# Kernel optimization log

Measured on AMD Instinct MI355X. Metric: run time of the kernel, lower is better.

The kernel has to match this reference:

```python
import math
import jax, jax.numpy as jnp
import numpy as np

EMBED_DIM = 1024
NUM_HEADS = 16
HEAD_DIM = EMBED_DIM // NUM_HEADS


def setup_inputs() -> dict:
    key = jax.random.key(0)
    ks = jax.random.split(key, 10)
    B, S, E = 2, 2048, EMBED_DIM
    x = jax.random.normal(ks[0], (B, S, E), dtype=jnp.float32)
    mask = jax.random.randint(ks[1], (B, S), 0, 2, dtype=jnp.int32)
    s = 1.0 / math.sqrt(E)
    Wq = jax.random.normal(ks[2], (E, E), dtype=jnp.float32) * s
    bq = jnp.zeros((E,), dtype=jnp.float32)
    Wk = jax.random.normal(ks[3], (E, E), dtype=jnp.float32) * s
    bk = jnp.zeros((E,), dtype=jnp.float32)
    Wv = jax.random.normal(ks[4], (E, E), dtype=jnp.float32) * s
    bv = jnp.zeros((E,), dtype=jnp.float32)
    Wo = jax.random.normal(ks[5], (E, E), dtype=jnp.float32) * s
    bo = jnp.zeros((E,), dtype=jnp.float32)
    return {"x": x, "mask": mask, "Wq": Wq, "bq": bq, "Wk": Wk, "bk": bk,
            "Wv": Wv, "bv": bv, "Wo": Wo, "bo": bo}


def reference(x, mask, Wq, bq, Wk, bk, Wv, bv, Wo, bo):
    B, S, E = x.shape
    H, D = NUM_HEADS, HEAD_DIM
    scale = math.sqrt(D)  # ScaledDotProductAttention built with head_dim

    def split_heads(t):
        return t.reshape(B, S, H, D).transpose(0, 2, 1, 3)  # [B,H,S,D]

    q = split_heads(x @ Wq + bq)
    k = split_heads(x @ Wk + bk)
    v = split_heads(x @ Wv + bv)

    scores = jnp.einsum('bhqd,bhkd->bhqk', q, k) / scale  # [B,H,S,S]
    m = mask[:, None, None, :].astype(scores.dtype)        # [B,1,1,S]
    neg = jnp.finfo(scores.dtype).min
    scores = jnp.where(m == 0, neg, scores)
    aw = jax.nn.softmax(scores, axis=-1)
    # post-softmax mask renormalization (as in the torch module)
    aw = aw * m
    denom = aw.sum(axis=-1, keepdims=True)
    aw = jnp.where(denom > 0, aw / jnp.where(denom > 0, denom, 1.0), 0.0)

    ctx = jnp.einsum('bhqk,bhkd->bhqd', aw, v)             # [B,H,S,D]
    ctx = ctx.transpose(0, 2, 1, 3).reshape(B, S, E)
    out = ctx @ Wo + bo
    return out
```

## Files before the change

### kernel.cpp

```cpp
#include <hip/hip_runtime.h>

typedef _Float16 half8 __attribute__((ext_vector_type(8)));
typedef _Float16 half4v __attribute__((ext_vector_type(4)));
typedef _Float16 h2 __attribute__((ext_vector_type(2)));
typedef float f4 __attribute__((ext_vector_type(4)));

#define ASYNC_COPY16(ldsp, gp)                                                     \
  __builtin_amdgcn_global_load_lds((__attribute__((address_space(1))) void*)(gp),  \
                                   (__attribute__((address_space(3))) void*)(ldsp),\
                                   16, 0, 0)

__device__ __forceinline__ f4 mfma16(half8 a, half8 b, f4 c) {
  return __builtin_amdgcn_mfma_f32_16x16x32_f16(a, b, c, 0, 0, 0);
}

__device__ __forceinline__ h2 pack2(float a, float b) {
  return __builtin_bit_cast(h2, __builtin_amdgcn_cvt_pkrtz(a, b));
}

#if defined(__has_builtin)
#if __has_builtin(__builtin_amdgcn_exp2f)
#define EXP2(x) __builtin_amdgcn_exp2f(x)
#endif
#if __has_builtin(__builtin_amdgcn_fdot2)
#define FDOT2(a, b, c) __builtin_amdgcn_fdot2((a), (b), (c), false)
#endif
#endif
#ifndef EXP2
#define EXP2(x) __expf((x) * 0.69314718056f)
#endif
#define KSCALE 0.18033688011f
#define FIXMAX 10.0f


__global__ __launch_bounds__(256) void k_cvt_x(const float* __restrict__ x,
                                               _Float16* __restrict__ xh) {
  int i = (blockIdx.x * 256 + threadIdx.x) * 4;
  f4 v = *(const f4*)(x + i);
  half4v h;
  h[0] = (_Float16)v[0]; h[1] = (_Float16)v[1];
  h[2] = (_Float16)v[2]; h[3] = (_Float16)v[3];
  *(half4v*)(xh + i) = h;
}

__global__ __launch_bounds__(256) void k_transpose_w(
    const float* __restrict__ Wq, const float* __restrict__ Wk,
    const float* __restrict__ Wv, const float* __restrict__ Wo,
    _Float16* __restrict__ wqkvT, _Float16* __restrict__ woT) {
  __shared__ float tw[32][33];
  int z = blockIdx.z;
  const float* w = (z == 0) ? Wq : (z == 1) ? Wk : (z == 2) ? Wv : Wo;
  _Float16* wt = (z == 3) ? woT : wqkvT + (size_t)z * 1048576;
  int k0 = blockIdx.y * 32, n0 = blockIdx.x * 32;
  int tx = threadIdx.x, ty = threadIdx.y;
  for (int j = 0; j < 32; j += 8) tw[ty + j][tx] = w[(size_t)(k0 + ty + j) * 1024 + n0 + tx];
  __syncthreads();
  for (int j = 0; j < 32; j += 8)
    wt[(size_t)(n0 + ty + j) * 1024 + k0 + tx] = (_Float16)tw[tx][ty + j];
}

__global__ __launch_bounds__(256) void k_gemm_proj(
    const _Float16* __restrict__ A, const _Float16* __restrict__ Bt,
    const float* __restrict__ bq, const float* __restrict__ bk, const float* __restrict__ bv,
    _Float16* __restrict__ Qo, _Float16* __restrict__ Ko, _Float16* __restrict__ Vto) {
  __shared__ __align__(16) _Float16 As[128 * 32];
  __shared__ __align__(16) _Float16 Bs[128 * 32];
  const int t = threadIdx.x, lane = t & 63, w = t >> 6;
  const int qd = lane >> 4, lr = lane & 15;
  const int m0 = blockIdx.y * 128, n0 = blockIdx.x * 128;
  const int wm = (w & 1) * 64, wn = (w >> 1) * 64;
  const f4 z4 = {0.f, 0.f, 0.f, 0.f};
  f4 acc[4][4];
#pragma unroll
  for (int i = 0; i < 4; ++i)
#pragma unroll
    for (int j = 0; j < 4; ++j) acc[i][j] = z4;

  const int c0 = t, c1 = t + 256;
  for (int k0 = 0; k0 < 1024; k0 += 32) {
    const _Float16* ga0 = A + (size_t)(m0 + (c0 >> 2)) * 1024 + k0 + (c0 & 3) * 8;
    const _Float16* ga1 = A + (size_t)(m0 + (c1 >> 2)) * 1024 + k0 + (c1 & 3) * 8;
    const _Float16* gb0 = Bt + (size_t)(n0 + (c0 >> 2)) * 1024 + k0 + (c0 & 3) * 8;
    const _Float16* gb1 = Bt + (size_t)(n0 + (c1 >> 2)) * 1024 + k0 + (c1 & 3) * 8;
    char* la = (char*)As + w * 1024;
    char* lb = (char*)Bs + w * 1024;
    ASYNC_COPY16(la, ga0);
    ASYNC_COPY16(la + 4096, ga1);
    ASYNC_COPY16(lb, gb0);
    ASYNC_COPY16(lb + 4096, gb1);
    __syncthreads();
    half8 af[4], bf[4];
#pragma unroll
    for (int i = 0; i < 4; ++i)
      af[i] = *(const half8*)(As + (wm + i * 16 + lr) * 32 + qd * 8);
#pragma unroll
    for (int j = 0; j < 4; ++j)
      bf[j] = *(const half8*)(Bs + (wn + j * 16 + lr) * 32 + qd * 8);
#pragma unroll
    for (int i = 0; i < 4; ++i)
#pragma unroll
      for (int j = 0; j < 4; ++j) acc[i][j] = mfma16(af[i], bf[j], acc[i][j]);
    __syncthreads();
  }

  const int mat = n0 >> 10;
  const float* bias = (mat == 0) ? bq : (mat == 1) ? bk : bv;
  if (mat == 2) {
#pragma unroll
    for (int i = 0; i < 4; ++i)
#pragma unroll
      for (int j = 0; j < 4; ++j) {
        int n = (n0 + wn + j * 16 + lr) & 1023;
        int hh = n >> 6, d = n & 63;
        int mb = m0 + wm + i * 16 + qd * 4;
        int bb = mb >> 11, sb = mb & 2047;
        float bval = bias[n];
        half4v hv;
#pragma unroll
        for (int r = 0; r < 4; ++r) hv[r] = (_Float16)(acc[i][j][r] + bval);
        *(half4v*)(Vto + ((size_t)(bb * 16 + hh) * 64 + d) * 2048 + sb) = hv;
      }
  } else {
    _Float16* outp = (mat == 0) ? Qo : Ko;
    const float scl = (mat == 0) ? KSCALE : 1.f;
#pragma unroll
    for (int i = 0; i < 4; ++i)
#pragma unroll
      for (int j = 0; j < 4; ++j)
#pragma unroll
        for (int r = 0; r < 4; ++r) {
          int m = m0 + wm + i * 16 + qd * 4 + r;
          int n = (n0 + wn + j * 16 + lr) & 1023;
          float v = (acc[i][j][r] + bias[n]) * scl;
          int bb = m >> 11, s = m & 2047, hh = n >> 6, d = n & 63;
          outp[(size_t)((bb * 16 + hh) * 2048 + s) * 64 + d] = (_Float16)v;
        }
  }
}

__global__ __launch_bounds__(256, 2) void k_attn(
    const _Float16* __restrict__ Qg, const _Float16* __restrict__ Kg,
    const _Float16* __restrict__ Vtg, const int* __restrict__ maskg,
    _Float16* __restrict__ Op, float* __restrict__ ml) {
  __shared__ __align__(16) _Float16 Ks[64][72];
  __shared__ __align__(16) _Float16 Vts[64][72];
  __shared__ __align__(16) _Float16 Pq[4][16][72];
  __shared__ float Msk[64];

  const int bh = blockIdx.y;
  const int b = bh >> 4;
  const int q0 = blockIdx.x * 128;
  const int z = blockIdx.z;
  const int kb = z * 1024;
  const int t = threadIdx.x, lane = t & 63, w = t >> 6;
  const int qd = lane >> 4, lr = lane & 15;

  half8 qf[2][2];
#pragma unroll
  for (int rt = 0; rt < 2; ++rt)
#pragma unroll
    for (int ks = 0; ks < 2; ++ks)
      qf[rt][ks] = *(const half8*)(Qg + (size_t)(bh * 2048 + q0 + w * 32 + rt * 16 + lr) * 64 +
                                   ks * 32 + qd * 8);

  float l_i[2] = {0.f, 0.f};
  const f4 z4 = {0.f, 0.f, 0.f, 0.f};
  f4 O[2][4];
#pragma unroll
  for (int rt = 0; rt < 2; ++rt)
#pragma unroll
    for (int dt = 0; dt < 4; ++dt) O[rt][dt] = z4;

  const int sr0 = t >> 3, scc = (t & 7) * 8;
  const int sr1 = sr0 + 32;
  const _Float16* Kbase = Kg + (size_t)bh * 2048 * 64 + (size_t)kb * 64;
  const _Float16* Vtbase = Vtg + (size_t)bh * 64 * 2048 + kb;

  f4 kr0 = *(const f4*)(Kbase + (size_t)sr0 * 64 + scc);
  f4 kr1 = *(const f4*)(Kbase + (size_t)sr1 * 64 + scc);
  f4 vr0 = *(const f4*)(Vtbase + (size_t)sr0 * 2048 + scc);
  f4 vr1 = *(const f4*)(Vtbase + (size_t)sr1 * 2048 + scc);
  float mval = 0.f;
  if (t < 64) mval = maskg[b * 2048 + kb + t] ? -FIXMAX : -30010.f;

#if defined(FDOT2)
  const h2 one2 = {(_Float16)1.f, (_Float16)1.f};
#endif

  for (int it = 0; it < 16; ++it) {
    __syncthreads();
    *(f4*)&Ks[sr0][scc] = kr0;
    *(f4*)&Ks[sr1][scc] = kr1;
    *(f4*)&Vts[sr0][scc] = vr0;
    *(f4*)&Vts[sr1][scc] = vr1;
    if (t < 64) Msk[t] = mval;
    __syncthreads();

    if (it < 15) {
      int kk = (it + 1) * 64;
      kr0 = *(const f4*)(Kbase + (size_t)(kk + sr0) * 64 + scc);
      kr1 = *(const f4*)(Kbase + (size_t)(kk + sr1) * 64 + scc);
      vr0 = *(const f4*)(Vtbase + (size_t)sr0 * 2048 + kk + scc);
      vr1 = *(const f4*)(Vtbase + (size_t)sr1 * 2048 + kk + scc);
      if (t < 64) mval = maskg[b * 2048 + kb + kk + t] ? -FIXMAX : -30010.f;
    }

    f4 sc[2][4];
#pragma unroll
    for (int kt = 0; kt < 4; ++kt) {
      f4 mv = *(const f4*)&Msk[kt * 16 + qd * 4];
      sc[0][kt] = mv;
      sc[1][kt] = mv;
    }
#pragma unroll
    for (int kt = 0; kt < 4; ++kt) {
      half8 k0 = *(const half8*)&Ks[kt * 16 + lr][qd * 8];
      half8 k1 = *(const half8*)&Ks[kt * 16 + lr][32 + qd * 8];
      sc[0][kt] = mfma16(k0, qf[0][0], sc[0][kt]);
      sc[0][kt] = mfma16(k1, qf[0][1], sc[0][kt]);
      sc[1][kt] = mfma16(k0, qf[1][0], sc[1][kt]);
      sc[1][kt] = mfma16(k1, qf[1][1], sc[1][kt]);
    }

#pragma unroll
    for (int rt = 0; rt < 2; ++rt) {
      float s = 0.f;
#pragma unroll
      for (int kt = 0; kt < 4; ++kt) {
        float p0 = EXP2(sc[rt][kt][0]);
        float p1 = EXP2(sc[rt][kt][1]);
        float p2 = EXP2(sc[rt][kt][2]);
        float p3 = EXP2(sc[rt][kt][3]);
        h2 pa = pack2(p0, p1);
        h2 pb = pack2(p2, p3);
#if defined(FDOT2)
        s = FDOT2(pa, one2, s);
        s = FDOT2(pb, one2, s);
#else
        s += p0 + p1 + p2 + p3;
#endif
        half4v hv;
        hv.lo = pa;
        hv.hi = pb;
        *(half4v*)&Pq[w][lr][kt * 16 + qd * 4] = hv;
      }
      s += __shfl_xor(s, 16, 64);
      s += __shfl_xor(s, 32, 64);
      l_i[rt] += s;

      half8 bp0 = *(const half8*)&Pq[w][lr][qd * 8];
      half8 bp1 = *(const half8*)&Pq[w][lr][32 + qd * 8];
#pragma unroll
      for (int dt = 0; dt < 4; ++dt) {
        half8 va0 = *(const half8*)&Vts[dt * 16 + lr][qd * 8];
        half8 va1 = *(const half8*)&Vts[dt * 16 + lr][32 + qd * 8];
        O[rt][dt] = mfma16(va0, bp0, O[rt][dt]);
        O[rt][dt] = mfma16(va1, bp1, O[rt][dt]);
      }
    }
  }

#pragma unroll
  for (int rt = 0; rt < 2; ++rt) {
    int qrow = q0 + w * 32 + rt * 16 + lr;
    size_t rowi = (size_t)(z * 32 + bh) * 2048 + qrow;
    _Float16* op = Op + rowi * 64;
#pragma unroll
    for (int dt = 0; dt < 4; ++dt) {
      half4v hv;
#pragma unroll
      for (int r = 0; r < 4; ++r) hv[r] = (_Float16)O[rt][dt][r];
      *(half4v*)(op + dt * 16 + qd * 4) = hv;
    }
    if (qd == 0) ml[rowi] = l_i[rt];
  }
}

__global__ __launch_bounds__(256) void k_merge(const _Float16* __restrict__ Op,
                                               const float* __restrict__ ml,
                                               _Float16* __restrict__ ctx) {
  int idx = blockIdx.x * 256 + threadIdx.x;
  int d8 = (idx & 7) * 8;
  int h = (idx >> 3) & 15;
  int q = idx >> 7;
  int b = q >> 11, s = q & 2047;
  int bh = b * 16 + h;
  size_t r1 = (size_t)bh * 2048 + s;
  size_t r2 = (size_t)(32 + bh) * 2048 + s;
  float l1 = ml[r1], l2 = ml[r2];
  float inv = 1.f / fmaxf(l1 + l2, 1e-20f);
  half8 o1 = *(const half8*)(Op + r1 * 64 + d8);
  half8 o2 = *(const half8*)(Op + r2 * 64 + d8);
  half8 ho;
#pragma unroll
  for (int j = 0; j < 8; ++j)
    ho[j] = (_Float16)(((float)o1[j] + (float)o2[j]) * inv);
  *(half8*)(ctx + (size_t)q * 1024 + h * 64 + d8) = ho;
}

__global__ __launch_bounds__(256) void k_gemm_out(
    const _Float16* __restrict__ A, const _Float16* __restrict__ Bt,
    const float* __restrict__ bo, float* __restrict__ out) {
  __shared__ __align__(16) _Float16 As[64 * 32];
  __shared__ __align__(16) _Float16 Bs[128 * 32];
  const int t = threadIdx.x, lane = t & 63, w = t >> 6;
  const int qd = lane >> 4, lr = lane & 15;
  const int m0 = blockIdx.y * 64, n0 = blockIdx.x * 128;
  const int wm = (w & 1) * 32, wn = (w >> 1) * 64;
  const f4 z4 = {0.f, 0.f, 0.f, 0.f};
  f4 acc[2][4];
#pragma unroll
  for (int i = 0; i < 2; ++i)
#pragma unroll
    for (int j = 0; j < 4; ++j) acc[i][j] = z4;

  const int c0 = t, c1 = t + 256;
  for (int k0 = 0; k0 < 1024; k0 += 32) {
    const _Float16* ga = A + (size_t)(m0 + (t >> 2)) * 1024 + k0 + (t & 3) * 8;
    const _Float16* gb0 = Bt + (size_t)(n0 + (c0 >> 2)) * 1024 + k0 + (c0 & 3) * 8;
    const _Float16* gb1 = Bt + (size_t)(n0 + (c1 >> 2)) * 1024 + k0 + (c1 & 3) * 8;
    char* la = (char*)As + w * 1024;
    char* lb = (char*)Bs + w * 1024;
    ASYNC_COPY16(la, ga);
    ASYNC_COPY16(lb, gb0);
    ASYNC_COPY16(lb + 4096, gb1);
    __syncthreads();
    half8 af[2], bf[4];
#pragma unroll
    for (int i = 0; i < 2; ++i)
      af[i] = *(const half8*)(As + (wm + i * 16 + lr) * 32 + qd * 8);
#pragma unroll
    for (int j = 0; j < 4; ++j)
      bf[j] = *(const half8*)(Bs + (wn + j * 16 + lr) * 32 + qd * 8);
#pragma unroll
    for (int i = 0; i < 2; ++i)
#pragma unroll
      for (int j = 0; j < 4; ++j) acc[i][j] = mfma16(af[i], bf[j], acc[i][j]);
    __syncthreads();
  }
#pragma unroll
  for (int i = 0; i < 2; ++i)
#pragma unroll
    for (int j = 0; j < 4; ++j)
#pragma unroll
      for (int r = 0; r < 4; ++r) {
        int m = m0 + wm + i * 16 + qd * 4 + r;
        int n = n0 + wn + j * 16 + lr;
        out[(size_t)m * 1024 + n] = acc[i][j][r] + bo[n];
      }
}

extern "C" void kernel_launch(void* const* d_in, const int* in_sizes, int n_in,
                              void* d_out, int out_size, void* d_ws, size_t ws_size,
                              hipStream_t stream) {
  const float* x = (const float*)d_in[0];
  const int* mask = (const int*)d_in[1];
  const float* Wq = (const float*)d_in[2];
  const float* bq = (const float*)d_in[3];
  const float* Wk = (const float*)d_in[4];
  const float* bk = (const float*)d_in[5];
  const float* Wv = (const float*)d_in[6];
  const float* bv = (const float*)d_in[7];
  const float* Wo = (const float*)d_in[8];
  const float* bo = (const float*)d_in[9];
  float* out = (float*)d_out;
  char* ws = (char*)d_ws;
  const size_t MB = 1 << 20;

  _Float16* Oph   = (_Float16*)(ws + 0);
  _Float16* xh    = (_Float16*)(ws + 0);
  _Float16* wqkvT = (_Float16*)(ws + 8 * MB);
  _Float16* woT   = (_Float16*)(ws + 16 * MB);
  _Float16* Qh    = (_Float16*)(ws + 18 * MB);
  _Float16* ctxh  = (_Float16*)(ws + 18 * MB);
  _Float16* Kh    = (_Float16*)(ws + 26 * MB);
  _Float16* Vth   = (_Float16*)(ws + 34 * MB);
  float*    mlw   = (float*)   (ws + 42 * MB);

  k_cvt_x<<<dim3(4096), dim3(256), 0, stream>>>(x, xh);
  k_transpose_w<<<dim3(32, 32, 4), dim3(32, 8), 0, stream>>>(Wq, Wk, Wv, Wo, wqkvT, woT);
  k_gemm_proj<<<dim3(24, 32), dim3(256), 0, stream>>>(xh, wqkvT, bq, bk, bv, Qh, Kh, Vth);
  k_attn<<<dim3(16, 32, 2), dim3(256), 0, stream>>>(Qh, Kh, Vth, mask, Oph, mlw);
  k_merge<<<dim3(2048), dim3(256), 0, stream>>>(Oph, mlw, ctxh);
  k_gemm_out<<<dim3(8, 64), dim3(256), 0, stream>>>(ctxh, woT, bo, out);
}
```

Measured before the change: 205.8 us.

## Double attention query tile per block and merge prep kernels into one launch

Each attention workgroup now handles 256 query rows (64 per wave) instead of 128, so every K/V tile staged into LDS is reused across twice as many queries. This halves K/V global loads and the grid size. The x-conversion and weight-transpose kernels are also fused into a single launch to save one kernel launch. In exchange the attention grid drops to 512 blocks, which may underfill the GPU, and register pressure rises with the larger O accumulator.

Result: no change. 203.5 us (-1.1%).

```diff
diff --git a/kernel.cpp b/kernel.cpp
--- a/kernel.cpp
+++ b/kernel.cpp
@@ -33,26 +33,28 @@
 #define FIXMAX 10.0f
 
 
-__global__ __launch_bounds__(256) void k_cvt_x(const float* __restrict__ x,
-                                               _Float16* __restrict__ xh) {
-  int i = (blockIdx.x * 256 + threadIdx.x) * 4;
-  f4 v = *(const f4*)(x + i);
-  half4v h;
-  h[0] = (_Float16)v[0]; h[1] = (_Float16)v[1];
-  h[2] = (_Float16)v[2]; h[3] = (_Float16)v[3];
-  *(half4v*)(xh + i) = h;
-}
-
-__global__ __launch_bounds__(256) void k_transpose_w(
+__global__ __launch_bounds__(256) void k_prep(
+    const float* __restrict__ x, _Float16* __restrict__ xh,
     const float* __restrict__ Wq, const float* __restrict__ Wk,
     const float* __restrict__ Wv, const float* __restrict__ Wo,
     _Float16* __restrict__ wqkvT, _Float16* __restrict__ woT) {
   __shared__ float tw[32][33];
-  int z = blockIdx.z;
+  const int bid = blockIdx.x, t = threadIdx.x;
+  if (bid < 4096) {
+    int i = (bid * 256 + t) * 4;
+    f4 v = *(const f4*)(x + i);
+    half4v h;
+    h[0] = (_Float16)v[0]; h[1] = (_Float16)v[1];
+    h[2] = (_Float16)v[2]; h[3] = (_Float16)v[3];
+    *(half4v*)(xh + i) = h;
+    return;
+  }
+  const int idx = bid - 4096;
+  const int z = idx >> 10, rem = idx & 1023;
+  const int n0 = (rem & 31) * 32, k0 = (rem >> 5) * 32;
   const float* w = (z == 0) ? Wq : (z == 1) ? Wk : (z == 2) ? Wv : Wo;
   _Float16* wt = (z == 3) ? woT : wqkvT + (size_t)z * 1048576;
-  int k0 = blockIdx.y * 32, n0 = blockIdx.x * 32;
-  int tx = threadIdx.x, ty = threadIdx.y;
+  const int tx = t & 31, ty = t >> 5;
   for (int j = 0; j < 32; j += 8) tw[ty + j][tx] = w[(size_t)(k0 + ty + j) * 1024 + n0 + tx];
   __syncthreads();
   for (int j = 0; j < 32; j += 8)
@@ -149,25 +151,25 @@
 
   const int bh = blockIdx.y;
   const int b = bh >> 4;
-  const int q0 = blockIdx.x * 128;
+  const int q0 = blockIdx.x * 256;
   const int z = blockIdx.z;
   const int kb = z * 1024;
   const int t = threadIdx.x, lane = t & 63, w = t >> 6;
   const int qd = lane >> 4, lr = lane & 15;
 
-  half8 qf[2][2];
-#pragma unroll
-  for (int rt = 0; rt < 2; ++rt)
+  half8 qf[4][2];
+#pragma unroll
+  for (int rt = 0; rt < 4; ++rt)
 #pragma unroll
     for (int ks = 0; ks < 2; ++ks)
-      qf[rt][ks] = *(const half8*)(Qg + (size_t)(bh * 2048 + q0 + w * 32 + rt * 16 + lr) * 64 +
+      qf[rt][ks] = *(const half8*)(Qg + (size_t)(bh * 2048 + q0 + w * 64 + rt * 16 + lr) * 64 +
                                    ks * 32 + qd * 8);
 
-  float l_i[2] = {0.f, 0.f};
+  float l_i[4] = {0.f, 0.f, 0.f, 0.f};
   const f4 z4 = {0.f, 0.f, 0.f, 0.f};
-  f4 O[2][4];
-#pragma unroll
-  for (int rt = 0; rt < 2; ++rt)
+  f4 O[4][4];
+#pragma unroll
+  for (int rt = 0; rt < 4; ++rt)
 #pragma unroll
     for (int dt = 0; dt < 4; ++dt) O[rt][dt] = z4;
 
@@ -205,64 +207,69 @@
       if (t < 64) mval = maskg[b * 2048 + kb + kk + t] ? -FIXMAX : -30010.f;
     }
 
-    f4 sc[2][4];
-#pragma unroll
-    for (int kt = 0; kt < 4; ++kt) {
-      f4 mv = *(const f4*)&Msk[kt * 16 + qd * 4];
-      sc[0][kt] = mv;
-      sc[1][kt] = mv;
+#pragma unroll
+    for (int rtp = 0; rtp < 2; ++rtp) {
+      const int r0 = rtp * 2, r1 = rtp * 2 + 1;
+      f4 sc[2][4];
+#pragma unroll
+      for (int kt = 0; kt < 4; ++kt) {
+        f4 mv = *(const f4*)&Msk[kt * 16 + qd * 4];
+        sc[0][kt] = mv;
+        sc[1][kt] = mv;
+      }
+#pragma unroll
+      for (int kt = 0; kt < 4; ++kt) {
+        half8 k0 = *(const half8*)&Ks[kt * 16 + lr][qd * 8];
+        half8 k1 = *(const half8*)&Ks[kt * 16 + lr][32 + qd * 8];
+        sc[0][kt] = mfma16(k0, qf[r0][0], sc[0][kt]);
+        sc[0][kt] = mfma16(k1, qf[r0][1], sc[0][kt]);
+        sc[1][kt] = mfma16(k0, qf[r1][0], sc[1][kt]);
+        sc[1][kt] = mfma16(k1, qf[r1][1], sc[1][kt]);
+      }
+
+#pragma unroll
+      for (int rr = 0; rr < 2; ++rr) {
+        const int rt = rtp * 2 + rr;
+        float s = 0.f;
+#pragma unroll
+        for (int kt = 0; kt < 4; ++kt) {
+          float p0 = EXP2(sc[rr][kt][0]);
+          float p1 = EXP2(sc[rr][kt][1]);
+          float p2 = EXP2(sc[rr][kt][2]);
+          float p3 = EXP2(sc[rr][kt][3]);
+          h2 pa = pack2(p0, p1);
+          h2 pb = pack2(p2, p3);
+#if defined(FDOT2)
+          s = FDOT2(pa, one2, s);
+          s = FDOT2(pb, one2, s);
+#else
+          s += p0 + p1 + p2 + p3;
+#endif
+          half4v hv;
+          hv.lo = pa;
+          hv.hi = pb;
+          *(half4v*)&Pq[w][lr][kt * 16 + qd * 4] = hv;
+        }
+        s += __shfl_xor(s, 16, 64);
+        s += __shfl_xor(s, 32, 64);
+        l_i[rt] += s;
+
+        half8 bp0 = *(const half8*)&Pq[w][lr][qd * 8];
+        half8 bp1 = *(const half8*)&Pq[w][lr][32 + qd * 8];
+#pragma unroll
+        for (int dt = 0; dt < 4; ++dt) {
+          half8 va0 = *(const half8*)&Vts[dt * 16 + lr][qd * 8];
+          half8 va1 = *(const half8*)&Vts[dt * 16 + lr][32 + qd * 8];
+          O[rt][dt] = mfma16(va0, bp0, O[rt][dt]);
+          O[rt][dt] = mfma16(va1, bp1, O[rt][dt]);
+        }
+      }
     }
-#pragma unroll
-    for (int kt = 0; kt < 4; ++kt) {
-      half8 k0 = *(const half8*)&Ks[kt * 16 + lr][qd * 8];
-      half8 k1 = *(const half8*)&Ks[kt * 16 + lr][32 + qd * 8];
-      sc[0][kt] = mfma16(k0, qf[0][0], sc[0][kt]);
-      sc[0][kt] = mfma16(k1, qf[0][1], sc[0][kt]);
-      sc[1][kt] = mfma16(k0, qf[1][0], sc[1][kt]);
-      sc[1][kt] = mfma16(k1, qf[1][1], sc[1][kt]);
-    }
-
-#pragma unroll
-    for (int rt = 0; rt < 2; ++rt) {
-      float s = 0.f;
-#pragma unroll
-      for (int kt = 0; kt < 4; ++kt) {
-        float p0 = EXP2(sc[rt][kt][0]);
-        float p1 = EXP2(sc[rt][kt][1]);
-        float p2 = EXP2(sc[rt][kt][2]);
-        float p3 = EXP2(sc[rt][kt][3]);
-        h2 pa = pack2(p0, p1);
-        h2 pb = pack2(p2, p3);
-#if defined(FDOT2)
-        s = FDOT2(pa, one2, s);
-        s = FDOT2(pb, one2, s);
-#else
-        s += p0 + p1 + p2 + p3;
-#endif
-        half4v hv;
-        hv.lo = pa;
-        hv.hi = pb;
-        *(half4v*)&Pq[w][lr][kt * 16 + qd * 4] = hv;
-      }
-      s += __shfl_xor(s, 16, 64);
-      s += __shfl_xor(s, 32, 64);
-      l_i[rt] += s;
-
-      half8 bp0 = *(const half8*)&Pq[w][lr][qd * 8];
-      half8 bp1 = *(const half8*)&Pq[w][lr][32 + qd * 8];
-#pragma unroll
-      for (int dt = 0; dt < 4; ++dt) {
-        half8 va0 = *(const half8*)&Vts[dt * 16 + lr][qd * 8];
-        half8 va1 = *(const half8*)&Vts[dt * 16 + lr][32 + qd * 8];
-        O[rt][dt] = mfma16(va0, bp0, O[rt][dt]);
-        O[rt][dt] = mfma16(va1, bp1, O[rt][dt]);
-      }
-    }
-  }
-
-#pragma unroll
-  for (int rt = 0; rt < 2; ++rt) {
-    int qrow = q0 + w * 32 + rt * 16 + lr;
+  }
+
+#pragma unroll
+  for (int rt = 0; rt < 4; ++rt) {
+    int qrow = q0 + w * 64 + rt * 16 + lr;
     size_t rowi = (size_t)(z * 32 + bh) * 2048 + qrow;
     _Float16* op = Op + rowi * 64;
 #pragma unroll
@@ -377,10 +384,9 @@
   _Float16* Vth   = (_Float16*)(ws + 34 * MB);
   float*    mlw   = (float*)   (ws + 42 * MB);
 
-  k_cvt_x<<<dim3(4096), dim3(256), 0, stream>>>(x, xh);
-  k_transpose_w<<<dim3(32, 32, 4), dim3(32, 8), 0, stream>>>(Wq, Wk, Wv, Wo, wqkvT, woT);
+  k_prep<<<dim3(8192), dim3(256), 0, stream>>>(x, xh, Wq, Wk, Wv, Wo, wqkvT, woT);
   k_gemm_proj<<<dim3(24, 32), dim3(256), 0, stream>>>(xh, wqkvT, bq, bk, bv, Qh, Kh, Vth);
-  k_attn<<<dim3(16, 32, 2), dim3(256), 0, stream>>>(Qh, Kh, Vth, mask, Oph, mlw);
+  k_attn<<<dim3(8, 32, 2), dim3(256), 0, stream>>>(Qh, Kh, Vth, mask, Oph, mlw);
   k_merge<<<dim3(2048), dim3(256), 0, stream>>>(Oph, mlw, ctxh);
   k_gemm_out<<<dim3(8, 64), dim3(256), 0, stream>>>(ctxh, woT, bo, out);
 }
```
